# Optimization experiments

Hardware: AMD Instinct MI355X
Metric: run time of the kernel (lower is better)

The kernel has to match this reference:

```python
import jax, jax.numpy as jnp
import numpy as np

D_MODEL = 512
NHEAD = 8
HEAD_DIM = D_MODEL // NHEAD
DFF = 2048
RANK = 64
L = 1024
N = 8
EPS = 1e-5


def _layer_norm(x, g, b):
    m = jnp.mean(x, axis=-1, keepdims=True)
    v = jnp.mean(jnp.square(x - m), axis=-1, keepdims=True)
    return (x - m) * jax.lax.rsqrt(v + EPS) * g + b


def setup_inputs() -> dict:
    key = jax.random.key(0)
    ks = jax.random.split(key, 20)
    s = 1.0 / np.sqrt(D_MODEL)
    inp = {
        "q": jax.random.normal(ks[0], (L, N, D_MODEL), jnp.float32),
        "k": jax.random.normal(ks[1], (L, N, D_MODEL), jnp.float32),
        "v": jax.random.normal(ks[2], (L, N, D_MODEL), jnp.float32),
        # attention projections, stored (in, out) so x @ W
        "Wq": jax.random.normal(ks[3], (D_MODEL, D_MODEL), jnp.float32) * s,
        "bq": jnp.zeros((D_MODEL,), jnp.float32),
        "Wk": jax.random.normal(ks[4], (D_MODEL, D_MODEL), jnp.float32) * s,
        "bk": jnp.zeros((D_MODEL,), jnp.float32),
        "Wv": jax.random.normal(ks[5], (D_MODEL, D_MODEL), jnp.float32) * s,
        "bv": jnp.zeros((D_MODEL,), jnp.float32),
        "Wo": jax.random.normal(ks[6], (D_MODEL, D_MODEL), jnp.float32) * s,
        "bo": jnp.zeros((D_MODEL,), jnp.float32),
        "topk": jnp.float32(0.3),  # learned scalar, k = int(S * sigmoid(topk))
        "A1": jax.random.normal(ks[7], (D_MODEL, RANK), jnp.float32) * s,
        "B1": jax.random.normal(ks[8], (RANK, DFF), jnp.float32) / np.sqrt(RANK),
        "A2": jax.random.normal(ks[9], (DFF, RANK), jnp.float32) / np.sqrt(DFF),
        "B2": jax.random.normal(ks[10], (RANK, D_MODEL), jnp.float32) / np.sqrt(RANK),
        "g1": jnp.ones((D_MODEL,), jnp.float32),
        "be1": jnp.zeros((D_MODEL,), jnp.float32),
        "g2": jnp.ones((D_MODEL,), jnp.float32),
        "be2": jnp.zeros((D_MODEL,), jnp.float32),
    }
    return inp


def reference(q, k, v, Wq, bq, Wk, bk, Wv, bv, Wo, bo, topk,
              A1, B1, A2, B2, g1, be1, g2, be2):
    Lq, Nb, E = q.shape
    S = k.shape[0]
    H, Dh = NHEAD, HEAD_DIM

    # projections -> (N, L, H, Dh)
    qh = (q @ Wq + bq).reshape(Lq, Nb, H, Dh).transpose(1, 0, 2, 3)
    kh = (k @ Wk + bk).reshape(S, Nb, H, Dh).transpose(1, 0, 2, 3)
    vh = (v @ Wv + bv).reshape(S, Nb, H, Dh).transpose(1, 0, 2, 3)

    scores = jnp.einsum('nlhd,nshd->nlhs', qh, kh) / jnp.sqrt(jnp.float32(Dh))

    # dynamic top-k mask: keep the k = int(S * sigmoid(topk)) largest per row
    k_keep = (S * jax.nn.sigmoid(topk)).astype(jnp.int32)  # 588 for topk=0.3
    sorted_desc = jnp.sort(scores, axis=-1)[..., ::-1]
    idx = jnp.broadcast_to(k_keep - 1, scores.shape[:-1])[..., None]
    thresh = jnp.take_along_axis(sorted_desc, idx, axis=-1)  # k-th largest
    masked = jnp.where(scores >= thresh, scores, -jnp.inf)
    attn_w = jax.nn.softmax(masked, axis=-1)

    # note original flattens (d, h) order: 'nlhs,nshd->nldh' then view(L,N,E)
    ao = jnp.einsum('nlhs,nshd->nldh', attn_w, vh)
    ao = ao.transpose(1, 0, 2, 3).reshape(Lq, Nb, E)
    attn_out = ao @ Wo + bo

    src = _layer_norm(q + attn_out, g1, be1)
    ffn = jax.nn.relu(src @ A1 @ B1) @ A2 @ B2
    src = _layer_norm(src + ffn, g2, be2)
    return src
```

## Files before the change

kernel.cpp:

```cpp
#include <hip/hip_runtime.h>

typedef unsigned short u16;
typedef unsigned int u32;
typedef unsigned long long u64;
using s16x8 = __attribute__((ext_vector_type(8))) short;
using s16x4 = __attribute__((ext_vector_type(4))) short;
using u16x4 = __attribute__((ext_vector_type(4))) unsigned short;
using u32x4 = __attribute__((ext_vector_type(4))) unsigned int;
using f32x4 = __attribute__((ext_vector_type(4))) float;

__device__ __forceinline__ u16 f2bf(float f) {
  unsigned int u = __float_as_uint(f);
  u += 0x7FFFu + ((u >> 16) & 1u);
  return (u16)(u >> 16);
}
__device__ __forceinline__ float bf2f(u16 b) {
  return __uint_as_float(((u32)b) << 16);
}
__device__ __forceinline__ u32 pkbf(float a, float b) {
  u32 r;
  asm("v_cvt_pk_bf16_f32 %0, %1, %2" : "=v"(r) : "v"(a), "v"(b));
  return r;
}
__device__ __forceinline__ u64 cmp_ge(u32 key, u32 cand) {
  u64 m;
  asm("v_cmp_le_u32 %0, %1, %2" : "=s"(m) : "s"(cand), "v"(key));
  return m;
}
__device__ __forceinline__ u32 f2key(float f) {
  u32 u = __float_as_uint(f);
  u32 flip = (u32)((int)u >> 31) | 0x80000000u;
  return (u ^ flip) >> 16;
}
__device__ __forceinline__ float key2f(u32 k) {
  u32 t = k << 16;
  u32 msk = ((int)t < 0) ? 0x80000000u : 0xFFFF0000u;
  return __uint_as_float(t ^ msk);
}

__global__ __launch_bounds__(256) void prep_w(
    const float* __restrict__ Wq, const float* __restrict__ Wk, const float* __restrict__ Wv,
    const float* __restrict__ Wo, const float* __restrict__ A1, const float* __restrict__ B1,
    const float* __restrict__ A2, const float* __restrict__ B2,
    u16* __restrict__ WqT, u16* __restrict__ WkT, u16* __restrict__ WvT, u16* __restrict__ WoT,
    u16* __restrict__ A1T, u16* __restrict__ B1T, u16* __restrict__ A2T, u16* __restrict__ B2T) {
  __shared__ u16 t[64][68];
  int b = blockIdx.x, tid = threadIdx.x;
  const float* src; u16* dst; int base, R, C;
  if (b < 64)        { src = Wq; dst = WqT; base = 0;   R = 512;  C = 512; }
  else if (b < 128)  { src = Wk; dst = WkT; base = 64;  R = 512;  C = 512; }
  else if (b < 192)  { src = Wv; dst = WvT; base = 128; R = 512;  C = 512; }
  else if (b < 256)  { src = Wo; dst = WoT; base = 192; R = 512;  C = 512; }
  else if (b < 264)  { src = A1; dst = A1T; base = 256; R = 512;  C = 64;  }
  else if (b < 296)  { src = B1; dst = B1T; base = 264; R = 64;   C = 2048;}
  else if (b < 328)  { src = A2; dst = A2T; base = 296; R = 2048; C = 64;  }
  else               { src = B2; dst = B2T; base = 328; R = 64;   C = 512; }
  int ti = b - base;
  int tpr = C >> 6;
  int r0 = (ti / tpr) * 64, c0 = (ti % tpr) * 64;
#pragma unroll
  for (int i = 0; i < 4; ++i) {
    int r = i * 16 + (tid >> 4), c = (tid & 15) * 4;
    float4 f = *(const float4*)&src[(size_t)(r0 + r) * C + c0 + c];
    t[r][c] = f2bf(f.x); t[r][c + 1] = f2bf(f.y);
    t[r][c + 2] = f2bf(f.z); t[r][c + 3] = f2bf(f.w);
  }
  __syncthreads();
#pragma unroll
  for (int i = 0; i < 4; ++i) {
    int cc = i * 16 + (tid >> 4), rr = (tid & 15) * 4;
    u16x4 o;
    o[0] = t[rr][cc]; o[1] = t[rr + 1][cc]; o[2] = t[rr + 2][cc]; o[3] = t[rr + 3][cc];
    *(u16x4*)&dst[(size_t)(c0 + cc) * R + r0 + rr] = o;
  }
}

__global__ __launch_bounds__(256, 4) void qkv_fused(
    const float* __restrict__ q, const float* __restrict__ k, const float* __restrict__ v,
    const u16* __restrict__ WqT, const u16* __restrict__ WkT, const u16* __restrict__ WvT,
    const float* __restrict__ bq, const float* __restrict__ bk, const float* __restrict__ bv,
    u16* __restrict__ Qw, u16* __restrict__ Kw, u16* __restrict__ Vw) {
  __shared__ __align__(16) u16 As[128][72];
  __shared__ __align__(16) u16 Bs[128][72];
  const int z = blockIdx.z;
  const float* A = z == 0 ? q : (z == 1 ? k : v);
  const u16* Bt = z == 0 ? WqT : (z == 1 ? WkT : WvT);
  const float* bias = z == 0 ? bq : (z == 1 ? bk : bv);
  u16* outp = z == 0 ? Qw : (z == 1 ? Kw : Vw);

  const int tid = threadIdx.x;
  const int m0 = blockIdx.y * 128, n0 = blockIdx.x * 128;
  const int lane = tid & 63, wid = tid >> 6;
  const int l16 = lane & 15, hi = lane >> 4;
  const int wr = (wid >> 1) * 64, wc = (wid & 1) * 64;

  f32x4 acc[4][4];
#pragma unroll
  for (int i = 0; i < 4; ++i)
#pragma unroll
    for (int j = 0; j < 4; ++j) acc[i][j] = (f32x4){0.f, 0.f, 0.f, 0.f};

  for (int k0 = 0; k0 < 512; k0 += 64) {
    if (k0) __syncthreads();
#pragma unroll
    for (int i = 0; i < 4; ++i) {
      int idx = i * 256 + tid;
      int r = idx >> 3, cc = (idx & 7) * 8;
      float4 f0 = *(const float4*)&A[(size_t)(m0 + r) * 512 + k0 + cc];
      float4 f1 = *(const float4*)&A[(size_t)(m0 + r) * 512 + k0 + cc + 4];
      u32x4 pk;
      pk[0] = pkbf(f0.x, f0.y); pk[1] = pkbf(f0.z, f0.w);
      pk[2] = pkbf(f1.x, f1.y); pk[3] = pkbf(f1.z, f1.w);
      *(u32x4*)&As[r][cc] = pk;
      *(s16x8*)&Bs[r][cc] = *(const s16x8*)&Bt[(size_t)(n0 + r) * 512 + k0 + cc];
    }
    __syncthreads();
#pragma unroll
    for (int kk = 0; kk < 2; ++kk) {
      const int kb_ = kk * 32 + hi * 8;
      s16x8 af[4], bf[4];
#pragma unroll
      for (int mf = 0; mf < 4; ++mf) af[mf] = *(const s16x8*)&As[wr + mf * 16 + l16][kb_];
#pragma unroll
      for (int nf = 0; nf < 4; ++nf) bf[nf] = *(const s16x8*)&Bs[wc + nf * 16 + l16][kb_];
#pragma unroll
      for (int mf = 0; mf < 4; ++mf)
#pragma unroll
        for (int nf = 0; nf < 4; ++nf)
          acc[mf][nf] = __builtin_amdgcn_mfma_f32_16x16x32_bf16(af[mf], bf[nf], acc[mf][nf], 0, 0, 0);
    }
  }

#pragma unroll
  for (int mf = 0; mf < 4; ++mf)
#pragma unroll
    for (int nf = 0; nf < 4; ++nf)
#pragma unroll
      for (int i = 0; i < 4; ++i) {
        int row = m0 + wr + mf * 16 + hi * 4 + i;
        int col = n0 + wc + nf * 16 + l16;
        float val = acc[mf][nf][i] + bias[col];
        if (z == 0) val *= 0.18033688f;
        int l = row >> 3, n = row & 7, hh = col >> 6, d = col & 63;
        if (z < 2)
          outp[(((size_t)(n * 8 + hh) * 1024 + l) << 6) + d] = f2bf(val);
        else
          outp[((size_t)(n * 8 + hh) * 64 + d) * 1024 + l] = f2bf(val);
      }
}

__global__ __launch_bounds__(512, 8) void attn_kernel(const u16* __restrict__ Qw,
                                                      const u16* __restrict__ Kw,
                                                      const u16* __restrict__ Vw,
                                                      const float* __restrict__ topk,
                                                      u16* __restrict__ ao) {
  __shared__ __align__(16) u16 scb[16 * 1024];
  __shared__ __align__(16) u16 Qt[16][72];
  __shared__ float invs[16];
  const int tid = threadIdx.x, lane = tid & 63, wid = tid >> 6;
  const int l16 = lane & 15, hi = lane >> 4;
  const int mb = blockIdx.x, nh = blockIdx.y;

  const int kkeep = (int)(1024.f / (1.f + __expf(-topk[0])));

  if (tid < 256) {
    int r = tid >> 4, dc = (tid & 15) << 2;
    *(s16x4*)&Qt[r][dc] =
        *(const s16x4*)&Qw[((size_t)nh * 1024 + mb * 16 + r) * 64 + dc];
  }
  __syncthreads();

  {
    const u16* Kb = Kw + (size_t)nh * 1024 * 64;
    s16x8 bq0 = *(const s16x8*)&Qt[l16][hi * 8];
    s16x8 bq1 = *(const s16x8*)&Qt[l16][32 + hi * 8];
    const int s0 = wid * 128;
    const size_t kbase = (size_t)(s0 + l16) * 64 + hi * 8;
    s16x8 c0 = *(const s16x8*)&Kb[kbase];
    s16x8 c1 = *(const s16x8*)&Kb[kbase + 32];
    char* rowq = (char*)scb + l16 * 2048;
    const int Xq = (l16 & 7) << 4;
#pragma unroll
    for (int nf = 0; nf < 8; ++nf) {
      const size_t nb = kbase + (size_t)(nf < 7 ? nf + 1 : nf) * 1024;
      s16x8 n0_ = *(const s16x8*)&Kb[nb];
      s16x8 n1_ = *(const s16x8*)&Kb[nb + 32];
      f32x4 acc = {0.f, 0.f, 0.f, 0.f};
      acc = __builtin_amdgcn_mfma_f32_16x16x32_bf16(c0, bq0, acc, 0, 0, 0);
      acc = __builtin_amdgcn_mfma_f32_16x16x32_bf16(c1, bq1, acc, 0, 0, 0);
      u32 k0 = f2key(acc[0]) | (f2key(acc[1]) << 16);
      u32 k1 = f2key(acc[2]) | (f2key(acc[3]) << 16);
      int boff = (2 * (s0 + nf * 16 + 4 * hi)) ^ Xq;
      *(uint2*)(rowq + boff) = make_uint2(k0, k1);
      c0 = n0_; c1 = n1_;
    }
  }
  __syncthreads();

  for (int rp = 0; rp < 2; ++rp) {
    const int r = wid * 2 + rp;
    char* rb = (char*)scb + r * 2048;
    const int X = (r & 7) << 4;
    const int oa = (16 * lane) ^ X, ob = (16 * lane + 1024) ^ X;
    u32x4 qa = *(const u32x4*)(rb + oa), qb_ = *(const u32x4*)(rb + ob);
    u32 ka[16];
#pragma unroll
    for (int j = 0; j < 4; ++j) {
      ka[2 * j] = qa[j] & 0xFFFFu; ka[2 * j + 1] = qa[j] >> 16;
      ka[8 + 2 * j] = qb_[j] & 0xFFFFu; ka[9 + 2 * j] = qb_[j] >> 16;
    }
    u32 T = 0;
    for (int bit = 15; bit >= 0; --bit) {
      u32 c = T + (1u << bit);
      int n = 0;
#pragma unroll
      for (int j = 0; j < 16; ++j) n += __builtin_popcountll(cmp_ge(ka[j], c));
      T = (n >= kkeep) ? c : T;
    }
    const float tv = key2f(T);
    float s = 0.f;
    u32x4 wa, wb;
#pragma unroll
    for (int j = 0; j < 4; ++j) {
      float e0 = (ka[2 * j] >= T) ? __builtin_amdgcn_exp2f(key2f(ka[2 * j]) - tv) : 0.f;
      float e1 = (ka[2 * j + 1] >= T) ? __builtin_amdgcn_exp2f(key2f(ka[2 * j + 1]) - tv) : 0.f;
      float e2 = (ka[8 + 2 * j] >= T) ? __builtin_amdgcn_exp2f(key2f(ka[8 + 2 * j]) - tv) : 0.f;
      float e3 = (ka[9 + 2 * j] >= T) ? __builtin_amdgcn_exp2f(key2f(ka[9 + 2 * j]) - tv) : 0.f;
      s += e0 + e1 + e2 + e3;
      wa[j] = pkbf(e0, e1); wb[j] = pkbf(e2, e3);
    }
    *(u32x4*)(rb + oa) = wa; *(u32x4*)(rb + ob) = wb;
#pragma unroll
    for (int off = 1; off < 64; off <<= 1) s += __shfl_xor(s, off);
    if (lane == 0) invs[r] = __builtin_amdgcn_rcpf(s);
  }
  __syncthreads();

  if (wid < 4) {
    const u16* Vb = Vw + (size_t)nh * 64 * 1024;
    const int d0 = wid * 16;
    f32x4 oacc0 = {0.f, 0.f, 0.f, 0.f};
    f32x4 oacc1 = {0.f, 0.f, 0.f, 0.f};
    const char* Pbase = (const char*)scb + l16 * 2048;
    const int Xp = (l16 & 7) << 4;
    const size_t vbase = (size_t)(d0 + l16) * 1024 + hi * 8;
    s16x8 v0 = *(const s16x8*)&Vb[vbase];
    s16x8 v1 = *(const s16x8*)&Vb[vbase + 32];
#pragma unroll
    for (int ks = 0; ks < 32; ks += 2) {
      const int kss = ks < 30 ? ks + 2 : ks;
      s16x8 nv0 = *(const s16x8*)&Vb[vbase + (size_t)kss * 32];
      s16x8 nv1 = *(const s16x8*)&Vb[vbase + (size_t)(kss + 1) * 32];
      s16x8 a0 = *(const s16x8*)(Pbase + ((ks * 64 + hi * 16) ^ Xp));
      s16x8 a1 = *(const s16x8*)(Pbase + (((ks + 1) * 64 + hi * 16) ^ Xp));
      oacc0 = __builtin_amdgcn_mfma_f32_16x16x32_bf16(a0, v0, oacc0, 0, 0, 0);
      oacc1 = __builtin_amdgcn_mfma_f32_16x16x32_bf16(a1, v1, oacc1, 0, 0, 0);
      v0 = nv0; v1 = nv1;
    }
    const int n = nh >> 3, hh = nh & 7;
#pragma unroll
    for (int i = 0; i < 4; ++i) {
      int l = mb * 16 + hi * 4 + i;
      int d = d0 + l16;
      float vv = (oacc0[i] + oacc1[i]) * invs[hi * 4 + i];
      ao[(size_t)(l * 8 + n) * 512 + d * 8 + hh] = f2bf(vv);
    }
  }
}

template <bool FIRST>
__global__ __launch_bounds__(256, 2) void gemm_ln(const u16* __restrict__ A,
                                                  const u16* __restrict__ Bt,
                                                  const float* __restrict__ bias,
                                                  const float* __restrict__ residf,
                                                  const u16* __restrict__ residb,
                                                  const float* __restrict__ g,
                                                  const float* __restrict__ be,
                                                  float* __restrict__ outf,
                                                  u16* __restrict__ outb) {
  constexpr int K = FIRST ? 512 : 64;
  __shared__ __align__(16) u16 As[16][72];
  __shared__ float red_s[4][16];
  __shared__ float red_q[4][16];
  const int tid = threadIdx.x;
  const int lane = tid & 63, wid = tid >> 6;
  const int l16 = lane & 15, hi = lane >> 4;
  const int m0 = blockIdx.x * 16;
  const int wc = wid * 128;

  f32x4 acc[8];
#pragma unroll
  for (int nf = 0; nf < 8; ++nf) acc[nf] = (f32x4){0.f, 0.f, 0.f, 0.f};

  for (int k0 = 0; k0 < K; k0 += 64) {
    if (k0) __syncthreads();
    {
      int r = tid >> 4, c = (tid & 15) << 2;
      *(s16x4*)&As[r][c] = *(const s16x4*)&A[(size_t)(m0 + r) * K + k0 + c];
    }
    __syncthreads();
#pragma unroll
    for (int kk = 0; kk < 2; ++kk) {
      const int kb_ = kk * 32 + hi * 8;
      s16x8 a = *(const s16x8*)&As[l16][kb_];
#pragma unroll
      for (int nf = 0; nf < 8; ++nf) {
        s16x8 b = *(const s16x8*)&Bt[(size_t)(wc + nf * 16 + l16) * K + k0 + kb_];
        acc[nf] = __builtin_amdgcn_mfma_f32_16x16x32_bf16(a, b, acc[nf], 0, 0, 0);
      }
    }
  }

#pragma unroll
  for (int nf = 0; nf < 8; ++nf) {
    int col = wc + nf * 16 + l16;
#pragma unroll
    for (int i = 0; i < 4; ++i) {
      float v = acc[nf][i];
      int row = m0 + hi * 4 + i;
      if (FIRST) v += bias[col] + residf[(size_t)row * 512 + col];
      else v += bf2f(residb[(size_t)row * 512 + col]);
      acc[nf][i] = v;
    }
  }
  float s[4] = {0.f, 0.f, 0.f, 0.f}, q2[4] = {0.f, 0.f, 0.f, 0.f};
#pragma unroll
  for (int nf = 0; nf < 8; ++nf)
#pragma unroll
    for (int i = 0; i < 4; ++i) {
      s[i] += acc[nf][i];
      q2[i] += acc[nf][i] * acc[nf][i];
    }
#pragma unroll
  for (int i = 0; i < 4; ++i) {
#pragma unroll
    for (int off = 1; off < 16; off <<= 1) {
      s[i] += __shfl_xor(s[i], off);
      q2[i] += __shfl_xor(q2[i], off);
    }
  }
  if (l16 == 0) {
#pragma unroll
    for (int i = 0; i < 4; ++i) {
      red_s[wid][hi * 4 + i] = s[i];
      red_q[wid][hi * 4 + i] = q2[i];
    }
  }
  __syncthreads();
  float mean[4], rstd[4];
#pragma unroll
  for (int i = 0; i < 4; ++i) {
    int r = hi * 4 + i;
    float ms = red_s[0][r] + red_s[1][r] + red_s[2][r] + red_s[3][r];
    float mq = red_q[0][r] + red_q[1][r] + red_q[2][r] + red_q[3][r];
    mean[i] = ms * (1.f / 512.f);
    float var = mq * (1.f / 512.f) - mean[i] * mean[i];
    rstd[i] = rsqrtf(var + 1e-5f);
  }
#pragma unroll
  for (int nf = 0; nf < 8; ++nf) {
    int col = wc + nf * 16 + l16;
    float gv = g[col], bev = be[col];
#pragma unroll
    for (int i = 0; i < 4; ++i) {
      int row = m0 + hi * 4 + i;
      float y = (acc[nf][i] - mean[i]) * rstd[i] * gv + bev;
      if (FIRST) outb[(size_t)row * 512 + col] = f2bf(y);
      else outf[(size_t)row * 512 + col] = y;
    }
  }
}

__global__ __launch_bounds__(256, 4) void ffn3(const u16* __restrict__ srcb,
                                               const u16* __restrict__ A1T,
                                               const u16* __restrict__ B1T,
                                               const u16* __restrict__ A2T,
                                               u16* __restrict__ w2) {
  __shared__ __align__(16) u16 As[32][72];
  __shared__ __align__(16) u16 Bs[64][72];
  __shared__ __align__(16) u16 Us[32][72];
  __shared__ __align__(16) u16 B1s[64][72];
  __shared__ __align__(16) u16 A2s[64][72];
  __shared__ __align__(16) u16 Hs[32][72];
  const int tid = threadIdx.x;
  const int lane = tid & 63, wid = tid >> 6;
  const int l16 = lane & 15, hi = lane >> 4;
  const int m0 = blockIdx.x * 32;
  const int wm = (wid & 1) * 16, wn = (wid >> 1) * 32;

  f32x4 accu[2];
  accu[0] = (f32x4){0.f, 0.f, 0.f, 0.f};
  accu[1] = (f32x4){0.f, 0.f, 0.f, 0.f};
  for (int k0 = 0; k0 < 512; k0 += 64) {
    if (k0) __syncthreads();
    {
      int r = tid >> 3, c = (tid & 7) << 3;
      *(s16x8*)&As[r][c] = *(const s16x8*)&srcb[(size_t)(m0 + r) * 512 + k0 + c];
    }
#pragma unroll
    for (int i = 0; i < 2; ++i) {
      int idx = i * 256 + tid;
      int r = idx >> 3, c = (idx & 7) << 3;
      *(s16x8*)&Bs[r][c] = *(const s16x8*)&A1T[(size_t)r * 512 + k0 + c];
    }
    __syncthreads();
#pragma unroll
    for (int kk = 0; kk < 2; ++kk) {
      const int kb_ = kk * 32 + hi * 8;
      s16x8 a = *(const s16x8*)&As[wm + l16][kb_];
#pragma unroll
      for (int j = 0; j < 2; ++j) {
        s16x8 b = *(const s16x8*)&Bs[wn + j * 16 + l16][kb_];
        accu[j] = __builtin_amdgcn_mfma_f32_16x16x32_bf16(a, b, accu[j], 0, 0, 0);
      }
    }
  }
  __syncthreads();
#pragma unroll
  for (int j = 0; j < 2; ++j)
#pragma unroll
    for (int i = 0; i < 4; ++i)
      Us[wm + hi * 4 + i][wn + j * 16 + l16] = f2bf(accu[j][i]);

  f32x4 w2a[2];
  w2a[0] = (f32x4){0.f, 0.f, 0.f, 0.f};
  w2a[1] = (f32x4){0.f, 0.f, 0.f, 0.f};
  for (int jc = 0; jc < 32; ++jc) {
#pragma unroll
    for (int i = 0; i < 2; ++i) {
      int idx = i * 256 + tid;
      int r = idx >> 3, c = (idx & 7) << 3;
      *(s16x8*)&B1s[r][c] = *(const s16x8*)&B1T[(size_t)(jc * 64 + r) * 64 + c];
      *(s16x8*)&A2s[r][c] = *(const s16x8*)&A2T[(size_t)r * 2048 + jc * 64 + c];
    }
    __syncthreads();
    f32x4 ha[2];
    ha[0] = (f32x4){0.f, 0.f, 0.f, 0.f};
    ha[1] = (f32x4){0.f, 0.f, 0.f, 0.f};
#pragma unroll
    for (int kk = 0; kk < 2; ++kk) {
      const int kb_ = kk * 32 + hi * 8;
      s16x8 a = *(const s16x8*)&Us[wm + l16][kb_];
#pragma unroll
      for (int j = 0; j < 2; ++j) {
        s16x8 b = *(const s16x8*)&B1s[wn + j * 16 + l16][kb_];
        ha[j] = __builtin_amdgcn_mfma_f32_16x16x32_bf16(a, b, ha[j], 0, 0, 0);
      }
    }
#pragma unroll
    for (int j = 0; j < 2; ++j)
#pragma unroll
      for (int i = 0; i < 4; ++i)
        Hs[wm + hi * 4 + i][wn + j * 16 + l16] = f2bf(fmaxf(ha[j][i], 0.f));
    __syncthreads();
#pragma unroll
    for (int kk = 0; kk < 2; ++kk) {
      const int kb_ = kk * 32 + hi * 8;
      s16x8 a = *(const s16x8*)&Hs[wm + l16][kb_];
#pragma unroll
      for (int j = 0; j < 2; ++j) {
        s16x8 b = *(const s16x8*)&A2s[wn + j * 16 + l16][kb_];
        w2a[j] = __builtin_amdgcn_mfma_f32_16x16x32_bf16(a, b, w2a[j], 0, 0, 0);
      }
    }
    __syncthreads();
  }
#pragma unroll
  for (int j = 0; j < 2; ++j)
#pragma unroll
    for (int i = 0; i < 4; ++i)
      w2[(size_t)(m0 + wm + hi * 4 + i) * 64 + wn + j * 16 + l16] = f2bf(w2a[j][i]);
}

extern "C" void kernel_launch(void* const* d_in, const int* in_sizes, int n_in,
                              void* d_out, int out_size, void* d_ws, size_t ws_size,
                              hipStream_t stream) {
  const float* q = (const float*)d_in[0];
  const float* k = (const float*)d_in[1];
  const float* v = (const float*)d_in[2];
  const float* Wq = (const float*)d_in[3];
  const float* bq = (const float*)d_in[4];
  const float* Wk = (const float*)d_in[5];
  const float* bk = (const float*)d_in[6];
  const float* Wv = (const float*)d_in[7];
  const float* bv = (const float*)d_in[8];
  const float* Wo = (const float*)d_in[9];
  const float* bo = (const float*)d_in[10];
  const float* topk = (const float*)d_in[11];
  const float* A1 = (const float*)d_in[12];
  const float* B1 = (const float*)d_in[13];
  const float* A2 = (const float*)d_in[14];
  const float* B2 = (const float*)d_in[15];
  const float* g1 = (const float*)d_in[16];
  const float* be1 = (const float*)d_in[17];
  const float* g2 = (const float*)d_in[18];
  const float* be2 = (const float*)d_in[19];

  char* ws = (char*)d_ws;
  constexpr size_t SZ_TOK_BF = (size_t)8192 * 512 * 2;
  constexpr size_t SZ_W_BF = (size_t)512 * 512 * 2;
  constexpr size_t O_QW = 0;
  constexpr size_t O_KW = O_QW + SZ_TOK_BF;
  constexpr size_t O_VW = O_KW + SZ_TOK_BF;
  constexpr size_t O_WQT = O_VW + SZ_TOK_BF;
  constexpr size_t O_WKT = O_WQT + SZ_W_BF;
  constexpr size_t O_WVT = O_WKT + SZ_W_BF;
  constexpr size_t O_WOT = O_WVT + SZ_W_BF;
  constexpr size_t O_A1T = O_WOT + SZ_W_BF;
  constexpr size_t O_B1T = O_A1T + 65536;
  constexpr size_t O_A2T = O_B1T + 262144;
  constexpr size_t O_B2T = O_A2T + 262144;
  constexpr size_t O_AO = O_B2T + 65536;
  constexpr size_t O_SRCB = O_AO + SZ_TOK_BF;
  constexpr size_t O_W2 = O_SRCB + SZ_TOK_BF;

  u16* Qw_ = (u16*)(ws + O_QW);
  u16* Kw_ = (u16*)(ws + O_KW);
  u16* Vw_ = (u16*)(ws + O_VW);
  u16* WqT = (u16*)(ws + O_WQT);
  u16* WkT = (u16*)(ws + O_WKT);
  u16* WvT = (u16*)(ws + O_WVT);
  u16* WoT = (u16*)(ws + O_WOT);
  u16* A1T = (u16*)(ws + O_A1T);
  u16* B1T = (u16*)(ws + O_B1T);
  u16* A2T = (u16*)(ws + O_A2T);
  u16* B2T = (u16*)(ws + O_B2T);
  u16* ao = (u16*)(ws + O_AO);
  u16* srcb = (u16*)(ws + O_SRCB);
  u16* w2 = (u16*)(ws + O_W2);

  prep_w<<<336, 256, 0, stream>>>(Wq, Wk, Wv, Wo, A1, B1, A2, B2,
                                  WqT, WkT, WvT, WoT, A1T, B1T, A2T, B2T);

  qkv_fused<<<dim3(4, 64, 3), 256, 0, stream>>>(q, k, v, WqT, WkT, WvT,
                                                bq, bk, bv, Qw_, Kw_, Vw_);

  attn_kernel<<<dim3(64, 64), 512, 0, stream>>>(Qw_, Kw_, Vw_, topk, ao);

  gemm_ln<true><<<512, 256, 0, stream>>>(ao, WoT, bo, q, nullptr, g1, be1, nullptr, srcb);

  ffn3<<<256, 256, 0, stream>>>(srcb, A1T, B1T, A2T, w2);

  gemm_ln<false><<<512, 256, 0, stream>>>(w2, B2T, nullptr, nullptr, srcb, g2, be2,
                                          (float*)d_out, nullptr);
}
```

Before: 258.8 us.

## Split FFN hidden dimension across four blocks and reduce partials in final GEMM

```diff
diff --git a/kernel.cpp b/kernel.cpp
--- a/kernel.cpp
+++ b/kernel.cpp
@@ -43,10 +43,11 @@
     const float* __restrict__ Wo, const float* __restrict__ A1, const float* __restrict__ B1,
     const float* __restrict__ A2, const float* __restrict__ B2,
     u16* __restrict__ WqT, u16* __restrict__ WkT, u16* __restrict__ WvT, u16* __restrict__ WoT,
-    u16* __restrict__ A1T, u16* __restrict__ B1T, u16* __restrict__ A2T, u16* __restrict__ B2T) {
+    u16* __restrict__ A1T, u16* __restrict__ B1T, u16* __restrict__ A2T, u16* __restrict__ B2T4) {
   __shared__ u16 t[64][68];
   int b = blockIdx.x, tid = threadIdx.x;
   const float* src; u16* dst; int base, R, C;
+  bool is_b2 = false;
   if (b < 64)        { src = Wq; dst = WqT; base = 0;   R = 512;  C = 512; }
   else if (b < 128)  { src = Wk; dst = WkT; base = 64;  R = 512;  C = 512; }
   else if (b < 192)  { src = Wv; dst = WvT; base = 128; R = 512;  C = 512; }
@@ -54,7 +55,7 @@
   else if (b < 264)  { src = A1; dst = A1T; base = 256; R = 512;  C = 64;  }
   else if (b < 296)  { src = B1; dst = B1T; base = 264; R = 64;   C = 2048;}
   else if (b < 328)  { src = A2; dst = A2T; base = 296; R = 2048; C = 64;  }
-  else               { src = B2; dst = B2T; base = 328; R = 64;   C = 512; }
+  else               { src = B2; dst = B2T4; base = 328; R = 64;  C = 512; is_b2 = true; }
   int ti = b - base;
   int tpr = C >> 6;
   int r0 = (ti / tpr) * 64, c0 = (ti % tpr) * 64;
@@ -71,7 +72,13 @@
     int cc = i * 16 + (tid >> 4), rr = (tid & 15) * 4;
     u16x4 o;
     o[0] = t[rr][cc]; o[1] = t[rr + 1][cc]; o[2] = t[rr + 2][cc]; o[3] = t[rr + 3][cc];
-    *(u16x4*)&dst[(size_t)(c0 + cc) * R + r0 + rr] = o;
+    if (is_b2) {
+#pragma unroll
+      for (int rep = 0; rep < 4; ++rep)
+        *(u16x4*)&dst[(size_t)(c0 + cc) * 256 + rep * 64 + r0 + rr] = o;
+    } else {
+      *(u16x4*)&dst[(size_t)(c0 + cc) * R + r0 + rr] = o;
+    }
   }
 }
 
@@ -278,7 +285,7 @@
                                                   const float* __restrict__ be,
                                                   float* __restrict__ outf,
                                                   u16* __restrict__ outb) {
-  constexpr int K = FIRST ? 512 : 64;
+  constexpr int K = FIRST ? 512 : 256;
   __shared__ __align__(16) u16 As[16][72];
   __shared__ float red_s[4][16];
   __shared__ float red_q[4][16];
@@ -375,7 +382,7 @@
                                                const u16* __restrict__ A1T,
                                                const u16* __restrict__ B1T,
                                                const u16* __restrict__ A2T,
-                                               u16* __restrict__ w2) {
+                                               u16* __restrict__ w2p) {
   __shared__ __align__(16) u16 As[32][72];
   __shared__ __align__(16) u16 Bs[64][72];
   __shared__ __align__(16) u16 Us[32][72];
@@ -386,6 +393,7 @@
   const int lane = tid & 63, wid = tid >> 6;
   const int l16 = lane & 15, hi = lane >> 4;
   const int m0 = blockIdx.x * 32;
+  const int jcg = blockIdx.y;
   const int wm = (wid & 1) * 16, wn = (wid >> 1) * 32;
 
   f32x4 accu[2];
@@ -425,7 +433,8 @@
   f32x4 w2a[2];
   w2a[0] = (f32x4){0.f, 0.f, 0.f, 0.f};
   w2a[1] = (f32x4){0.f, 0.f, 0.f, 0.f};
-  for (int jc = 0; jc < 32; ++jc) {
+  for (int jt = 0; jt < 8; ++jt) {
+    const int jc = jcg * 8 + jt;
 #pragma unroll
     for (int i = 0; i < 2; ++i) {
       int idx = i * 256 + tid;
@@ -469,7 +478,7 @@
   for (int j = 0; j < 2; ++j)
 #pragma unroll
     for (int i = 0; i < 4; ++i)
-      w2[(size_t)(m0 + wm + hi * 4 + i) * 64 + wn + j * 16 + l16] = f2bf(w2a[j][i]);
+      w2p[(size_t)(m0 + wm + hi * 4 + i) * 256 + jcg * 64 + wn + j * 16 + l16] = f2bf(w2a[j][i]);
 }
 
 extern "C" void kernel_launch(void* const* d_in, const int* in_sizes, int n_in,
@@ -509,10 +518,10 @@
   constexpr size_t O_A1T = O_WOT + SZ_W_BF;
   constexpr size_t O_B1T = O_A1T + 65536;
   constexpr size_t O_A2T = O_B1T + 262144;
-  constexpr size_t O_B2T = O_A2T + 262144;
-  constexpr size_t O_AO = O_B2T + 65536;
+  constexpr size_t O_B2T4 = O_A2T + 262144;
+  constexpr size_t O_AO = O_B2T4 + 262144;
   constexpr size_t O_SRCB = O_AO + SZ_TOK_BF;
-  constexpr size_t O_W2 = O_SRCB + SZ_TOK_BF;
+  constexpr size_t O_W2P = O_SRCB + SZ_TOK_BF;
 
   u16* Qw_ = (u16*)(ws + O_QW);
   u16* Kw_ = (u16*)(ws + O_KW);
@@ -524,13 +533,13 @@
   u16* A1T = (u16*)(ws + O_A1T);
   u16* B1T = (u16*)(ws + O_B1T);
   u16* A2T = (u16*)(ws + O_A2T);
-  u16* B2T = (u16*)(ws + O_B2T);
+  u16* B2T4 = (u16*)(ws + O_B2T4);
   u16* ao = (u16*)(ws + O_AO);
   u16* srcb = (u16*)(ws + O_SRCB);
-  u16* w2 = (u16*)(ws + O_W2);
+  u16* w2p = (u16*)(ws + O_W2P);
 
   prep_w<<<336, 256, 0, stream>>>(Wq, Wk, Wv, Wo, A1, B1, A2, B2,
-                                  WqT, WkT, WvT, WoT, A1T, B1T, A2T, B2T);
+                                  WqT, WkT, WvT, WoT, A1T, B1T, A2T, B2T4);
 
   qkv_fused<<<dim3(4, 64, 3), 256, 0, stream>>>(q, k, v, WqT, WkT, WvT,
                                                 bq, bk, bv, Qw_, Kw_, Vw_);
@@ -539,8 +548,8 @@
 
   gemm_ln<true><<<512, 256, 0, stream>>>(ao, WoT, bo, q, nullptr, g1, be1, nullptr, srcb);
 
-  ffn3<<<256, 256, 0, stream>>>(srcb, A1T, B1T, A2T, w2);
-
-  gemm_ln<false><<<512, 256, 0, stream>>>(w2, B2T, nullptr, nullptr, srcb, g2, be2,
+  ffn3<<<dim3(256, 4), 256, 0, stream>>>(srcb, A1T, B1T, A2T, w2p);
+
+  gemm_ln<false><<<512, 256, 0, stream>>>(w2p, B2T4, nullptr, nullptr, srcb, g2, be2,
                                           (float*)d_out, nullptr);
 }
```

Measured after the change: 260.6 us. About the same (+0.7%).
